# Optimization experiments

Hardware: AMD Instinct MI355X
Metric: run time of the kernel (lower is better)

## Reference

```python
import jax, jax.numpy as jnp
import numpy as np

B, N, D_IN, D_OUT = 8, 2048, 256, 256
BN_EPS = 1e-5
SELU_ALPHA = 1.6732632423543772
SELU_SCALE = 1.0507009873554805


def setup_inputs() -> dict:
    key = jax.random.key(0)
    k1, k2, k3, k4 = jax.random.split(key, 4)
    lim_lin = 1.0 / np.sqrt(D_IN)
    return {
        "x": jax.random.normal(k1, (B, N, D_IN), dtype=jnp.float32),
        "w_map": jax.random.uniform(k2, (D_IN,), jnp.float32, -lim_lin, lim_lin),
        "w_att": jax.random.uniform(k3, (D_OUT, D_IN), jnp.float32, -lim_lin, lim_lin),
        "w_res": jax.random.uniform(k4, (D_OUT, D_IN), jnp.float32, -lim_lin, lim_lin),
        "gamma": jnp.ones((D_OUT,), jnp.float32),
        "beta": jnp.zeros((D_OUT,), jnp.float32),
    }


def _selu(x):
    x_clamped = jnp.clip(x, -10.0, 10.0)
    return SELU_SCALE * jnp.where(x > 0, x, SELU_ALPHA * (jnp.exp(x_clamped) - 1.0))


def reference(x, w_map, w_att, w_res, gamma, beta):
    # scores[b,i,j] = sum_d w_map[d] * x[b,i,d] * x[b,j,d]  (== W_map(x_i*x_j))
    scores = jnp.einsum("bid,bjd->bij", x * w_map, x)  # [B,N,N]
    attn = jax.nn.softmax(scores, axis=-1)
    aggregated = jnp.einsum("bij,bjd->bid", attn, x)  # [B,N,D]
    out = aggregated @ w_att.T + x @ w_res.T  # [B,N,D_OUT]
    # BatchNorm1d in training mode: stats over (batch, nodes) per channel, biased var
    mean = jnp.mean(out, axis=(0, 1))
    var = jnp.mean(jnp.square(out - mean), axis=(0, 1))
    out = (out - mean) * jax.lax.rsqrt(var + BN_EPS) * gamma + beta
    return _selu(out)
```

## Files before the change

kernel.cpp:

```cpp
#include <hip/hip_runtime.h>
#include <hip/hip_bf16.h>


typedef __attribute__((ext_vector_type(8)))  short bf16x8;
typedef __attribute__((ext_vector_type(4)))  float f32x4;
typedef __attribute__((ext_vector_type(16))) float f32x16;

#define MFMA16(a, b, c) __builtin_amdgcn_mfma_f32_16x16x32_bf16((a), (b), (c), 0, 0, 0)
#define MFMA32(a, b, c) __builtin_amdgcn_mfma_f32_32x32x16_bf16((a), (b), (c), 0, 0, 0)

constexpr int   NB = 8, NN = 2048;
constexpr int   ROWS = NB * NN;
constexpr float BN_EPS = 1e-5f;
constexpr float SELU_ALPHA = 1.6732632423543772f;
constexpr float SELU_SCALE = 1.0507009873554805f;

__device__ __forceinline__ unsigned short f2bf(float f) {
  union { float f; unsigned int u; } v; v.f = f;
  unsigned int u = v.u;
  u += 0x7FFFu + ((u >> 16) & 1u);
  return (unsigned short)(u >> 16);
}
__device__ __forceinline__ float bf2f(unsigned short h) {
  union { float f; unsigned int u; } v; v.u = ((unsigned int)h) << 16;
  return v.f;
}
__device__ __forceinline__ unsigned int pk2(float lo, float hi) {
  return (unsigned int)f2bf(lo) | ((unsigned int)f2bf(hi) << 16);
}

__device__ __forceinline__ void async_copy16(const unsigned short* g, unsigned short* l) {
  __builtin_amdgcn_global_load_lds(
      (const __attribute__((address_space(1))) void*)g,
      (__attribute__((address_space(3))) void*)l, 16, 0, 0);
}

__global__ __launch_bounds__(256) void k0_prep(const float* __restrict__ x,
                                               unsigned short* __restrict__ XR,
                                               unsigned short* __restrict__ Xt,
                                               const float* __restrict__ w_att,
                                               const float* __restrict__ w_res,
                                               unsigned short* __restrict__ WC,
                                               float* __restrict__ sums) {
  __shared__ unsigned short Ls[64 * 264];
  const int t = threadIdx.x;
  const int b = blockIdx.x & 7, rt = blockIdx.x >> 3;
  const int grb = b * NN + rt * 64;
  const int c = (t & 31) * 8, r0 = t >> 5;
#pragma unroll
  for (int q = 0; q < 8; ++q) {
    int r = r0 + q * 8;
    const float* xp = x + (size_t)(grb + r) * 256 + c;
    float4 a = *(const float4*)xp;
    float4 d = *(const float4*)(xp + 4);
    union { unsigned short s[8]; uint4 v; } xb;
    xb.s[0] = f2bf(a.x); xb.s[1] = f2bf(a.y); xb.s[2] = f2bf(a.z); xb.s[3] = f2bf(a.w);
    xb.s[4] = f2bf(d.x); xb.s[5] = f2bf(d.y); xb.s[6] = f2bf(d.z); xb.s[7] = f2bf(d.w);
    *(uint4*)(XR + (size_t)(grb + r) * 256 + c) = xb.v;
    *(uint4*)&Ls[r * 264 + c] = xb.v;
  }
  __syncthreads();
  unsigned short* dst = Xt + ((size_t)b * 256 + t) * 2048 + rt * 64;
#pragma unroll
  for (int k = 0; k < 8; ++k) {
    union { unsigned short s[8]; uint4 v; } o;
#pragma unroll
    for (int j = 0; j < 8; ++j) o.s[j] = Ls[(k * 8 + j) * 264 + t];
    *(uint4*)(dst + k * 8) = o.v;
  }
  if (blockIdx.x == 0 && t < 256) ((float4*)sums)[t] = make_float4(0.f, 0.f, 0.f, 0.f);
  if (blockIdx.x < 64) {
    int f = (blockIdx.x * 256 + t) * 8;
    int cc = f >> 9, k = f & 511;
    const float* src = (k < 256) ? (w_att + cc * 256 + k) : (w_res + cc * 256 + (k - 256));
    float4 a = *(const float4*)src;
    float4 d = *(const float4*)(src + 4);
    union { unsigned short s[8]; uint4 v; } o;
    o.s[0] = f2bf(a.x); o.s[1] = f2bf(a.y); o.s[2] = f2bf(a.z); o.s[3] = f2bf(a.w);
    o.s[4] = f2bf(d.x); o.s[5] = f2bf(d.y); o.s[6] = f2bf(d.z); o.s[7] = f2bf(d.w);
    *(uint4*)(WC + f) = o.v;
  }
}

__global__ __launch_bounds__(512, 2) void k1_attn(const float* __restrict__ w_map,
                                                  const unsigned short* __restrict__ XR,
                                                  const unsigned short* __restrict__ Xt,
                                                  unsigned short* __restrict__ Opart,
                                                  float* __restrict__ Lpart) {
  __shared__ unsigned short Ks[2][32 * 256];
  __shared__ unsigned short Vt[2][256 * 32];

  const int t = threadIdx.x;
  const int w = t >> 6, lane = t & 63;
  const int l31 = lane & 31, h = lane >> 5;
  const int qb = blockIdx.x >> 2, p = blockIdx.x & 3;
  const int b = qb >> 3;
  const int rowbase = qb * 256;
  const int jb0 = b * 2048 + p * 512;
  const unsigned short* Xtb = Xt + (size_t)b * 256 * 2048;

  int kSrc[2], vSrc[2];
#pragma unroll
  for (int q = 0; q < 2; ++q) {
    int cch = q * 512 + t;
    int kj = cch >> 5, kck = cch & 31;
    int pj = ((kj >> 3) & 1) * 16 + ((kj >> 4) & 1) * 4 + (kj & 3) + ((kj >> 2) & 1) * 8;
    kSrc[q] = (jb0 + pj) * 256 + ((kck ^ (kj & 7)) * 8);
    int vd = cch >> 2, vcj = cch & 3;
    vSrc[q] = vd * 2048 + p * 512 + ((vcj ^ ((vd >> 1) & 3)) * 8);
  }

#pragma unroll
  for (int q = 0; q < 2; ++q)
    async_copy16(XR + kSrc[q], &Ks[0][(q * 512 + t) * 8]);
#pragma unroll
  for (int q = 0; q < 2; ++q)
    async_copy16(Xtb + vSrc[q], &Vt[0][(q * 512 + t) * 8]);

  bf16x8 qf[16];
  {
    const unsigned short* xrow = XR + (size_t)(rowbase + w * 32 + l31) * 256 + h * 8;
#pragma unroll
    for (int kc = 0; kc < 16; ++kc) {
      bf16x8 xb = *(const bf16x8*)(xrow + kc * 16);
      const float* wp = w_map + kc * 16 + h * 8;
      float4 w0 = *(const float4*)wp, w1 = *(const float4*)(wp + 4);
      float wv[8] = {w0.x, w0.y, w0.z, w0.w, w1.x, w1.y, w1.z, w1.w};
      bf16x8 qv;
#pragma unroll
      for (int i = 0; i < 8; ++i)
        qv[i] = (short)f2bf(bf2f((unsigned short)xb[i]) * wv[i]);
      qf[kc] = qv;
    }
  }

  const f32x16 fz16 = {0.f,0.f,0.f,0.f, 0.f,0.f,0.f,0.f, 0.f,0.f,0.f,0.f, 0.f,0.f,0.f,0.f};
  f32x16 oacc[8];
#pragma unroll
  for (int i = 0; i < 8; ++i) oacc[i] = fz16;
  float rsum = 0.f;

  const int sw7 = l31 & 7;
  const int vkey = (l31 >> 1) & 3;

  for (int jt = 0; jt < 16; ++jt) {
    const int cur = jt & 1;
    __syncthreads();
    if (jt < 15) {
#pragma unroll
      for (int q = 0; q < 2; ++q)
        async_copy16(XR + kSrc[q] + (jt + 1) * 8192, &Ks[cur ^ 1][(q * 512 + t) * 8]);
#pragma unroll
      for (int q = 0; q < 2; ++q)
        async_copy16(Xtb + vSrc[q] + (jt + 1) * 32, &Vt[cur ^ 1][(q * 512 + t) * 8]);
    }
    f32x16 sA = fz16, sB = fz16;
#pragma unroll
    for (int kc = 0; kc < 8; ++kc) {
      bf16x8 kf = *(const bf16x8*)&Ks[cur][l31 * 256 + (((2 * kc + h) ^ sw7) * 8)];
      sA = MFMA32(kf, qf[kc], sA);
    }
#pragma unroll
    for (int kc = 8; kc < 16; ++kc) {
      bf16x8 kf = *(const bf16x8*)&Ks[cur][l31 * 256 + (((2 * kc + h) ^ sw7) * 8)];
      sB = MFMA32(kf, qf[kc], sB);
    }
    float pv[16];
#pragma unroll
    for (int r = 0; r < 16; ++r) {
      pv[r] = __expf(sA[r] + sB[r]);
      rsum += pv[r];
    }
    union { unsigned int u[4]; bf16x8 v; } a0, a1;
    a0.u[0] = pk2(pv[0],  pv[1]);
    a0.u[1] = pk2(pv[2],  pv[3]);
    a0.u[2] = pk2(pv[8],  pv[9]);
    a0.u[3] = pk2(pv[10], pv[11]);
    a1.u[0] = pk2(pv[4],  pv[5]);
    a1.u[1] = pk2(pv[6],  pv[7]);
    a1.u[2] = pk2(pv[12], pv[13]);
    a1.u[3] = pk2(pv[14], pv[15]);
#pragma unroll
    for (int dt = 0; dt < 8; ++dt) {
      const int dbase = (dt * 32 + l31) * 32;
      bf16x8 v0 = *(const bf16x8*)&Vt[cur][dbase + ((h ^ vkey) * 8)];
      oacc[dt] = MFMA32(a0.v, v0, oacc[dt]);
      bf16x8 v1 = *(const bf16x8*)&Vt[cur][dbase + (((2 + h) ^ vkey) * 8)];
      oacc[dt] = MFMA32(a1.v, v1, oacc[dt]);
    }
  }

  float rsT = rsum + __shfl_xor(rsum, 32);
  if (h == 0) Lpart[(size_t)p * ROWS + rowbase + w * 32 + l31] = rsT;
  unsigned short* ob = Opart + ((size_t)p * ROWS + rowbase + w * 32) * 256 + l31;
#pragma unroll
  for (int dt = 0; dt < 8; ++dt)
#pragma unroll
    for (int r = 0; r < 16; ++r) {
      int qrow = (r & 3) + ((r >> 2) << 3) + (h << 2);
      ob[qrow * 256 + dt * 32] = f2bf(oacc[dt][r]);
    }
}

__global__ __launch_bounds__(256) void kc_comb(const unsigned short* __restrict__ Opart,
                                               const float* __restrict__ Lpart,
                                               unsigned short* __restrict__ Oagg) {
  const int t = threadIdx.x;
  const int row = blockIdx.x * 8 + (t >> 5);
  const int col = (t & 31) * 8;
  const float invL = 1.0f / (Lpart[row] + Lpart[ROWS + row] +
                             Lpart[2 * ROWS + row] + Lpart[3 * ROWS + row]);
  const size_t base = (size_t)row * 256 + col;
  union { unsigned short s[8]; uint4 v; } p0, p1, p2, p3, o;
  p0.v = *(const uint4*)(Opart + base);
  p1.v = *(const uint4*)(Opart + (size_t)ROWS * 256 + base);
  p2.v = *(const uint4*)(Opart + (size_t)2 * ROWS * 256 + base);
  p3.v = *(const uint4*)(Opart + (size_t)3 * ROWS * 256 + base);
#pragma unroll
  for (int e = 0; e < 8; ++e)
    o.s[e] = f2bf(((bf2f(p0.s[e]) + bf2f(p1.s[e])) + (bf2f(p2.s[e]) + bf2f(p3.s[e]))) * invL);
  *(uint4*)(Oagg + base) = o.v;
}

__global__ __launch_bounds__(256, 2) void k2_gemm(const unsigned short* __restrict__ XR,
                                                  const unsigned short* __restrict__ Oagg,
                                                  const unsigned short* __restrict__ WC,
                                                  float* __restrict__ out,
                                                  float* __restrict__ sums) {
  __shared__ unsigned short As[128 * 72];
  __shared__ unsigned short Bs[64 * 72];
  __shared__ float cs[64], cq[64];
  const int t = threadIdx.x;
  const int w = t >> 6, lane = t & 63, l15 = lane & 15, quad = lane >> 4;
  const int m0 = (blockIdx.x >> 2) * 128, n0 = (blockIdx.x & 3) * 64;
  if (t < 64) { cs[t] = 0.f; cq[t] = 0.f; }

  const f32x4 fz = {0.f, 0.f, 0.f, 0.f};
  f32x4 acc[4][2];
#pragma unroll
  for (int i = 0; i < 4; ++i) { acc[i][0] = fz; acc[i][1] = fz; }

  for (int kk = 0; kk < 512; kk += 64) {
    __syncthreads();
#pragma unroll
    for (int q = 0; q < 4; ++q) {
      int idx = t + q * 256;
      int row = idx >> 3, koff = (idx & 7) * 8;
      const unsigned short* src = (kk < 256)
          ? (Oagg + (size_t)(m0 + row) * 256 + kk + koff)
          : (XR + (size_t)(m0 + row) * 256 + (kk - 256) + koff);
      *(uint4*)&As[row * 72 + koff] = *(const uint4*)src;
    }
#pragma unroll
    for (int q = 0; q < 2; ++q) {
      int idx = t + q * 256;
      int row = idx >> 3, koff = (idx & 7) * 8;
      *(uint4*)&Bs[row * 72 + koff] = *(const uint4*)(WC + (size_t)(n0 + row) * 512 + kk + koff);
    }
    __syncthreads();
#pragma unroll
    for (int kc = 0; kc < 2; ++kc) {
      bf16x8 b0 = *(const bf16x8*)&Bs[((w >> 1) * 32 + l15) * 72 + kc * 32 + quad * 8];
      bf16x8 b1 = *(const bf16x8*)&Bs[((w >> 1) * 32 + 16 + l15) * 72 + kc * 32 + quad * 8];
#pragma unroll
      for (int mt = 0; mt < 4; ++mt) {
        bf16x8 af = *(const bf16x8*)&As[((w & 1) * 64 + mt * 16 + l15) * 72 + kc * 32 + quad * 8];
        acc[mt][0] = MFMA16(af, b0, acc[mt][0]);
        acc[mt][1] = MFMA16(af, b1, acc[mt][1]);
      }
    }
  }
#pragma unroll
  for (int mt = 0; mt < 4; ++mt)
#pragma unroll
    for (int nt = 0; nt < 2; ++nt)
#pragma unroll
      for (int r = 0; r < 4; ++r) {
        int grow = m0 + (w & 1) * 64 + mt * 16 + quad * 4 + r;
        int gcol = n0 + (w >> 1) * 32 + nt * 16 + l15;
        out[(size_t)grow * 256 + gcol] = acc[mt][nt][r];
      }
#pragma unroll
  for (int nt = 0; nt < 2; ++nt) {
    float a = 0.f, b2 = 0.f;
#pragma unroll
    for (int mt = 0; mt < 4; ++mt)
#pragma unroll
      for (int r = 0; r < 4; ++r) {
        float v = acc[mt][nt][r];
        a += v; b2 += v * v;
      }
    a += __shfl_xor(a, 16);  a += __shfl_xor(a, 32);
    b2 += __shfl_xor(b2, 16); b2 += __shfl_xor(b2, 32);
    if (quad == 0) {
      int ci = (w >> 1) * 32 + nt * 16 + l15;
      atomicAdd(&cs[ci], a);
      atomicAdd(&cq[ci], b2);
    }
  }
  __syncthreads();
  if (t < 64) {
    atomicAdd(&sums[n0 + t], cs[t]);
    atomicAdd(&sums[256 + n0 + t], cq[t]);
  }
}

__global__ __launch_bounds__(256) void k4_bn_selu(float* __restrict__ out,
                                                  const float* __restrict__ sums,
                                                  const float* __restrict__ gamma,
                                                  const float* __restrict__ beta) {
  int f = (blockIdx.x * 256 + threadIdx.x) * 8;
  int c = f & 255;
  const float inv_m = 1.0f / 16384.0f;
  float4 v0 = *(const float4*)(out + f);
  float4 v1 = *(const float4*)(out + f + 4);
  float vv[8] = {v0.x, v0.y, v0.z, v0.w, v1.x, v1.y, v1.z, v1.w};
#pragma unroll
  for (int k = 0; k < 8; ++k) {
    int ch = c + k;
    float mean = sums[ch] * inv_m;
    float var = sums[256 + ch] * inv_m - mean * mean;
    float y = (vv[k] - mean) * rsqrtf(var + BN_EPS) * gamma[ch] + beta[ch];
    float yc = fminf(fmaxf(y, -10.f), 10.f);
    float r = (y > 0.f) ? y : (SELU_ALPHA * (expf(yc) - 1.0f));
    vv[k] = SELU_SCALE * r;
  }
  float4 o0 = {vv[0], vv[1], vv[2], vv[3]};
  float4 o1 = {vv[4], vv[5], vv[6], vv[7]};
  *(float4*)(out + f) = o0;
  *(float4*)(out + f + 4) = o1;
}

extern "C" void kernel_launch(void* const* d_in, const int* in_sizes, int n_in,
                              void* d_out, int out_size, void* d_ws, size_t ws_size,
                              hipStream_t stream) {
  const float* x     = (const float*)d_in[0];
  const float* w_map = (const float*)d_in[1];
  const float* w_att = (const float*)d_in[2];
  const float* w_res = (const float*)d_in[3];
  const float* gamma = (const float*)d_in[4];
  const float* beta  = (const float*)d_in[5];
  float* out = (float*)d_out;

  unsigned short* XR = (unsigned short*)d_ws;
  unsigned short* Xt = XR + (size_t)ROWS * 256;
  unsigned short* WC = Xt + (size_t)NB * 256 * 2048;
  unsigned short* Opart = WC + 256 * 512;
  float* Lpart = (float*)(Opart + (size_t)4 * ROWS * 256);
  float* sums  = Lpart + 4 * ROWS;
  unsigned short* Oagg = Xt;

  k0_prep<<<256, 256, 0, stream>>>(x, XR, Xt, w_att, w_res, WC, sums);
  k1_attn<<<256, 512, 0, stream>>>(w_map, XR, Xt, Opart, Lpart);
  kc_comb<<<2048, 256, 0, stream>>>(Opart, Lpart, Oagg);
  k2_gemm<<<512, 256, 0, stream>>>(XR, Oagg, WC, out, sums);
  k4_bn_selu<<<2048, 256, 0, stream>>>(out, sums, gamma, beta);
}
```

Before: 163.0 us.

## Fuse partial-combine and BatchNorm+SELU into GEMM with grid-wide barrier

Removes the separate combine kernel: the GEMM now sums the four attention partials and applies the 1/L normalisation while loading its A tile. It also removes the separate BN+SELU kernel by having every block publish column statistics with global atomics, wait at a grid-wide spin barrier on a counter, then normalise and apply SELU in registers before a single write of the output. This avoids writing and re-reading the aggregated activations and the fp32 pre-activation output, and drops two launches. The GEMM tile becomes 64 rows by all 256 columns, so W is reloaded per block. The spin barrier relies on all 256 blocks being co-resident and on the counter being reset before each call, which the visible code does not show.

After: 177.8 us. 1.09x slower.

```diff
diff --git a/kernel.cpp b/kernel.cpp
--- a/kernel.cpp
+++ b/kernel.cpp
@@ -202,86 +202,86 @@
     }
 }
 
-__global__ __launch_bounds__(256) void kc_comb(const unsigned short* __restrict__ Opart,
-                                               const float* __restrict__ Lpart,
-                                               unsigned short* __restrict__ Oagg) {
-  const int t = threadIdx.x;
-  const int row = blockIdx.x * 8 + (t >> 5);
-  const int col = (t & 31) * 8;
-  const float invL = 1.0f / (Lpart[row] + Lpart[ROWS + row] +
-                             Lpart[2 * ROWS + row] + Lpart[3 * ROWS + row]);
-  const size_t base = (size_t)row * 256 + col;
-  union { unsigned short s[8]; uint4 v; } p0, p1, p2, p3, o;
-  p0.v = *(const uint4*)(Opart + base);
-  p1.v = *(const uint4*)(Opart + (size_t)ROWS * 256 + base);
-  p2.v = *(const uint4*)(Opart + (size_t)2 * ROWS * 256 + base);
-  p3.v = *(const uint4*)(Opart + (size_t)3 * ROWS * 256 + base);
-#pragma unroll
-  for (int e = 0; e < 8; ++e)
-    o.s[e] = f2bf(((bf2f(p0.s[e]) + bf2f(p1.s[e])) + (bf2f(p2.s[e]) + bf2f(p3.s[e]))) * invL);
-  *(uint4*)(Oagg + base) = o.v;
-}
-
 __global__ __launch_bounds__(256, 2) void k2_gemm(const unsigned short* __restrict__ XR,
-                                                  const unsigned short* __restrict__ Oagg,
+                                                  const unsigned short* __restrict__ Opart,
+                                                  const float* __restrict__ Lpart,
                                                   const unsigned short* __restrict__ WC,
                                                   float* __restrict__ out,
-                                                  float* __restrict__ sums) {
-  __shared__ unsigned short As[128 * 72];
-  __shared__ unsigned short Bs[64 * 72];
-  __shared__ float cs[64], cq[64];
+                                                  float* __restrict__ sums,
+                                                  const float* __restrict__ gamma,
+                                                  const float* __restrict__ beta) {
+  __shared__ unsigned short As[64 * 72];
+  __shared__ unsigned short Bs[256 * 72];
+  __shared__ float invLs[64];
   const int t = threadIdx.x;
   const int w = t >> 6, lane = t & 63, l15 = lane & 15, quad = lane >> 4;
-  const int m0 = (blockIdx.x >> 2) * 128, n0 = (blockIdx.x & 3) * 64;
-  if (t < 64) { cs[t] = 0.f; cq[t] = 0.f; }
+  const int m0 = blockIdx.x * 64;
+  if (t < 64) {
+    int row = m0 + t;
+    invLs[t] = 1.0f / (Lpart[row] + Lpart[ROWS + row] +
+                       Lpart[2 * ROWS + row] + Lpart[3 * ROWS + row]);
+  }
 
   const f32x4 fz = {0.f, 0.f, 0.f, 0.f};
-  f32x4 acc[4][2];
-#pragma unroll
-  for (int i = 0; i < 4; ++i) { acc[i][0] = fz; acc[i][1] = fz; }
+  f32x4 acc[4][4];
+#pragma unroll
+  for (int i = 0; i < 4; ++i)
+#pragma unroll
+    for (int j = 0; j < 4; ++j) acc[i][j] = fz;
 
   for (int kk = 0; kk < 512; kk += 64) {
     __syncthreads();
-#pragma unroll
-    for (int q = 0; q < 4; ++q) {
-      int idx = t + q * 256;
+    if (kk < 256) {
+#pragma unroll
+      for (int i = 0; i < 2; ++i) {
+        int idx = t + i * 256;
+        int row = idx >> 3, koff = (idx & 7) * 8;
+        size_t base = (size_t)(m0 + row) * 256 + kk + koff;
+        union { unsigned short s[8]; uint4 v; } p0, p1, p2, p3, o;
+        p0.v = *(const uint4*)(Opart + base);
+        p1.v = *(const uint4*)(Opart + (size_t)ROWS * 256 + base);
+        p2.v = *(const uint4*)(Opart + (size_t)2 * ROWS * 256 + base);
+        p3.v = *(const uint4*)(Opart + (size_t)3 * ROWS * 256 + base);
+        float il = invLs[row];
+#pragma unroll
+        for (int e = 0; e < 8; ++e)
+          o.s[e] = f2bf(((bf2f(p0.s[e]) + bf2f(p1.s[e])) +
+                         (bf2f(p2.s[e]) + bf2f(p3.s[e]))) * il);
+        *(uint4*)&As[row * 72 + koff] = o.v;
+      }
+    } else {
+#pragma unroll
+      for (int i = 0; i < 2; ++i) {
+        int idx = t + i * 256;
+        int row = idx >> 3, koff = (idx & 7) * 8;
+        *(uint4*)&As[row * 72 + koff] =
+            *(const uint4*)(XR + (size_t)(m0 + row) * 256 + (kk - 256) + koff);
+      }
+    }
+#pragma unroll
+    for (int i = 0; i < 8; ++i) {
+      int idx = t + i * 256;
       int row = idx >> 3, koff = (idx & 7) * 8;
-      const unsigned short* src = (kk < 256)
-          ? (Oagg + (size_t)(m0 + row) * 256 + kk + koff)
-          : (XR + (size_t)(m0 + row) * 256 + (kk - 256) + koff);
-      *(uint4*)&As[row * 72 + koff] = *(const uint4*)src;
-    }
-#pragma unroll
-    for (int q = 0; q < 2; ++q) {
-      int idx = t + q * 256;
-      int row = idx >> 3, koff = (idx & 7) * 8;
-      *(uint4*)&Bs[row * 72 + koff] = *(const uint4*)(WC + (size_t)(n0 + row) * 512 + kk + koff);
+      *(uint4*)&Bs[row * 72 + koff] = *(const uint4*)(WC + (size_t)row * 512 + kk + koff);
     }
     __syncthreads();
 #pragma unroll
     for (int kc = 0; kc < 2; ++kc) {
-      bf16x8 b0 = *(const bf16x8*)&Bs[((w >> 1) * 32 + l15) * 72 + kc * 32 + quad * 8];
-      bf16x8 b1 = *(const bf16x8*)&Bs[((w >> 1) * 32 + 16 + l15) * 72 + kc * 32 + quad * 8];
-#pragma unroll
-      for (int mt = 0; mt < 4; ++mt) {
-        bf16x8 af = *(const bf16x8*)&As[((w & 1) * 64 + mt * 16 + l15) * 72 + kc * 32 + quad * 8];
-        acc[mt][0] = MFMA16(af, b0, acc[mt][0]);
-        acc[mt][1] = MFMA16(af, b1, acc[mt][1]);
-      }
-    }
-  }
-#pragma unroll
-  for (int mt = 0; mt < 4; ++mt)
-#pragma unroll
-    for (int nt = 0; nt < 2; ++nt)
-#pragma unroll
-      for (int r = 0; r < 4; ++r) {
-        int grow = m0 + (w & 1) * 64 + mt * 16 + quad * 4 + r;
-        int gcol = n0 + (w >> 1) * 32 + nt * 16 + l15;
-        out[(size_t)grow * 256 + gcol] = acc[mt][nt][r];
-      }
-#pragma unroll
-  for (int nt = 0; nt < 2; ++nt) {
+      bf16x8 af[4];
+#pragma unroll
+      for (int mt = 0; mt < 4; ++mt)
+        af[mt] = *(const bf16x8*)&As[(mt * 16 + l15) * 72 + kc * 32 + quad * 8];
+#pragma unroll
+      for (int nt = 0; nt < 4; ++nt) {
+        bf16x8 bf = *(const bf16x8*)&Bs[(w * 64 + nt * 16 + l15) * 72 + kc * 32 + quad * 8];
+#pragma unroll
+        for (int mt = 0; mt < 4; ++mt)
+          acc[mt][nt] = MFMA16(af[mt], bf, acc[mt][nt]);
+      }
+    }
+  }
+#pragma unroll
+  for (int nt = 0; nt < 4; ++nt) {
     float a = 0.f, b2 = 0.f;
 #pragma unroll
     for (int mt = 0; mt < 4; ++mt)
@@ -293,42 +293,41 @@
     a += __shfl_xor(a, 16);  a += __shfl_xor(a, 32);
     b2 += __shfl_xor(b2, 16); b2 += __shfl_xor(b2, 32);
     if (quad == 0) {
-      int ci = (w >> 1) * 32 + nt * 16 + l15;
-      atomicAdd(&cs[ci], a);
-      atomicAdd(&cq[ci], b2);
-    }
-  }
+      int col = w * 64 + nt * 16 + l15;
+      atomicAdd(&sums[col], a);
+      atomicAdd(&sums[256 + col], b2);
+    }
+  }
+  __threadfence();
   __syncthreads();
-  if (t < 64) {
-    atomicAdd(&sums[n0 + t], cs[t]);
-    atomicAdd(&sums[256 + n0 + t], cq[t]);
-  }
-}
-
-__global__ __launch_bounds__(256) void k4_bn_selu(float* __restrict__ out,
-                                                  const float* __restrict__ sums,
-                                                  const float* __restrict__ gamma,
-                                                  const float* __restrict__ beta) {
-  int f = (blockIdx.x * 256 + threadIdx.x) * 8;
-  int c = f & 255;
+  int* cnt = (int*)(sums + 512);
+  if (t == 0) {
+    atomicAdd(cnt, 1);
+    while (__hip_atomic_load(cnt, __ATOMIC_ACQUIRE, __HIP_MEMORY_SCOPE_AGENT) < 256)
+      __builtin_amdgcn_s_sleep(8);
+  }
+  __syncthreads();
   const float inv_m = 1.0f / 16384.0f;
-  float4 v0 = *(const float4*)(out + f);
-  float4 v1 = *(const float4*)(out + f + 4);
-  float vv[8] = {v0.x, v0.y, v0.z, v0.w, v1.x, v1.y, v1.z, v1.w};
-#pragma unroll
-  for (int k = 0; k < 8; ++k) {
-    int ch = c + k;
-    float mean = sums[ch] * inv_m;
-    float var = sums[256 + ch] * inv_m - mean * mean;
-    float y = (vv[k] - mean) * rsqrtf(var + BN_EPS) * gamma[ch] + beta[ch];
-    float yc = fminf(fmaxf(y, -10.f), 10.f);
-    float r = (y > 0.f) ? y : (SELU_ALPHA * (expf(yc) - 1.0f));
-    vv[k] = SELU_SCALE * r;
-  }
-  float4 o0 = {vv[0], vv[1], vv[2], vv[3]};
-  float4 o1 = {vv[4], vv[5], vv[6], vv[7]};
-  *(float4*)(out + f) = o0;
-  *(float4*)(out + f + 4) = o1;
+#pragma unroll
+  for (int nt = 0; nt < 4; ++nt) {
+    int col = w * 64 + nt * 16 + l15;
+    float sm = __hip_atomic_load(&sums[col], __ATOMIC_RELAXED, __HIP_MEMORY_SCOPE_AGENT);
+    float sq = __hip_atomic_load(&sums[256 + col], __ATOMIC_RELAXED, __HIP_MEMORY_SCOPE_AGENT);
+    float mean = sm * inv_m;
+    float var = sq * inv_m - mean * mean;
+    float sc = rsqrtf(var + BN_EPS) * gamma[col];
+    float bi = beta[col] - mean * sc;
+#pragma unroll
+    for (int mt = 0; mt < 4; ++mt)
+#pragma unroll
+      for (int r = 0; r < 4; ++r) {
+        int grow = m0 + mt * 16 + quad * 4 + r;
+        float y = acc[mt][nt][r] * sc + bi;
+        float yc = fminf(fmaxf(y, -10.f), 10.f);
+        float rr = (y > 0.f) ? y : (SELU_ALPHA * (expf(yc) - 1.0f));
+        out[(size_t)grow * 256 + col] = SELU_SCALE * rr;
+      }
+  }
 }
 
 extern "C" void kernel_launch(void* const* d_in, const int* in_sizes, int n_in,
@@ -348,11 +347,8 @@
   unsigned short* Opart = WC + 256 * 512;
   float* Lpart = (float*)(Opart + (size_t)4 * ROWS * 256);
   float* sums  = Lpart + 4 * ROWS;
-  unsigned short* Oagg = Xt;
 
   k0_prep<<<256, 256, 0, stream>>>(x, XR, Xt, w_att, w_res, WC, sums);
   k1_attn<<<256, 512, 0, stream>>>(w_map, XR, Xt, Opart, Lpart);
-  kc_comb<<<2048, 256, 0, stream>>>(Opart, Lpart, Oagg);
-  k2_gemm<<<512, 256, 0, stream>>>(XR, Oagg, WC, out, sums);
-  k4_bn_selu<<<2048, 256, 0, stream>>>(out, sums, gamma, beta);
-}
+  k2_gemm<<<256, 256, 0, stream>>>(XR, Opart, Lpart, WC, out, sums, gamma, beta);
+}
```

## Software-pipeline QK^T and PV across tiles with triple-buffered V in attention kernel

Applied to the files above, without the earlier changes.

Restructures the attention loop so the score MFMAs for tile j+1 are issued alongside the PV MFMAs for tile j, with the exp/pack of the new scores placed after the PV work. K stays double-buffered and V becomes triple-buffered, with a two-tile-ahead prefetch and a prologue/epilogue. The aim is to hide the exp/softmax latency and the MFMA dependency chains behind independent matrix work. The cost is more LDS (an extra V buffer), which may hurt occupancy at 2 blocks per CU, plus more live registers.

Result: slower. 172.6 us (+5.9%).

```diff
diff --git a/kernel.cpp b/kernel.cpp
--- a/kernel.cpp
+++ b/kernel.cpp
@@ -88,7 +88,7 @@
                                                   unsigned short* __restrict__ Opart,
                                                   float* __restrict__ Lpart) {
   __shared__ unsigned short Ks[2][32 * 256];
-  __shared__ unsigned short Vt[2][256 * 32];
+  __shared__ unsigned short Vt[3][256 * 32];
 
   const int t = threadIdx.x;
   const int w = t >> 6, lane = t & 63;
@@ -111,11 +111,15 @@
   }
 
 #pragma unroll
-  for (int q = 0; q < 2; ++q)
+  for (int q = 0; q < 2; ++q) {
     async_copy16(XR + kSrc[q], &Ks[0][(q * 512 + t) * 8]);
-#pragma unroll
-  for (int q = 0; q < 2; ++q)
+    async_copy16(XR + kSrc[q] + 8192, &Ks[1][(q * 512 + t) * 8]);
+  }
+#pragma unroll
+  for (int q = 0; q < 2; ++q) {
     async_copy16(Xtb + vSrc[q], &Vt[0][(q * 512 + t) * 8]);
+    async_copy16(Xtb + vSrc[q] + 32, &Vt[1][(q * 512 + t) * 8]);
+  }
 
   bf16x8 qf[16];
   {
@@ -143,50 +147,85 @@
   const int sw7 = l31 & 7;
   const int vkey = (l31 >> 1) & 3;
 
-  for (int jt = 0; jt < 16; ++jt) {
-    const int cur = jt & 1;
+  __syncthreads();
+
+  bf16x8 afA, afB;
+  {
+    f32x16 sA = fz16, sB = fz16;
+#pragma unroll
+    for (int kc = 0; kc < 8; ++kc) {
+      bf16x8 kf = *(const bf16x8*)&Ks[0][l31 * 256 + (((2 * kc + h) ^ sw7) * 8)];
+      sA = MFMA32(kf, qf[kc], sA);
+    }
+#pragma unroll
+    for (int kc = 8; kc < 16; ++kc) {
+      bf16x8 kf = *(const bf16x8*)&Ks[0][l31 * 256 + (((2 * kc + h) ^ sw7) * 8)];
+      sB = MFMA32(kf, qf[kc], sB);
+    }
+    float pv[16];
+#pragma unroll
+    for (int r = 0; r < 16; ++r) { pv[r] = __expf(sA[r] + sB[r]); rsum += pv[r]; }
+    union { unsigned int u[4]; bf16x8 v; } a0, a1;
+    a0.u[0] = pk2(pv[0],  pv[1]);  a0.u[1] = pk2(pv[2],  pv[3]);
+    a0.u[2] = pk2(pv[8],  pv[9]);  a0.u[3] = pk2(pv[10], pv[11]);
+    a1.u[0] = pk2(pv[4],  pv[5]);  a1.u[1] = pk2(pv[6],  pv[7]);
+    a1.u[2] = pk2(pv[12], pv[13]); a1.u[3] = pk2(pv[14], pv[15]);
+    afA = a0.v; afB = a1.v;
+  }
+
+  int v_cur = 0, v_nxt = 1, v_dma = 2;
+
+  for (int jt = 0; jt < 15; ++jt) {
     __syncthreads();
-    if (jt < 15) {
+    if (jt < 14) {
 #pragma unroll
       for (int q = 0; q < 2; ++q)
-        async_copy16(XR + kSrc[q] + (jt + 1) * 8192, &Ks[cur ^ 1][(q * 512 + t) * 8]);
+        async_copy16(XR + kSrc[q] + (jt + 2) * 8192, &Ks[jt & 1][(q * 512 + t) * 8]);
 #pragma unroll
       for (int q = 0; q < 2; ++q)
-        async_copy16(Xtb + vSrc[q] + (jt + 1) * 32, &Vt[cur ^ 1][(q * 512 + t) * 8]);
-    }
+        async_copy16(Xtb + vSrc[q] + (jt + 2) * 32, &Vt[v_dma][(q * 512 + t) * 8]);
+    }
+    const unsigned short* Kb = &Ks[(jt + 1) & 1][0];
     f32x16 sA = fz16, sB = fz16;
 #pragma unroll
     for (int kc = 0; kc < 8; ++kc) {
-      bf16x8 kf = *(const bf16x8*)&Ks[cur][l31 * 256 + (((2 * kc + h) ^ sw7) * 8)];
+      bf16x8 kf = *(const bf16x8*)&Kb[l31 * 256 + (((2 * kc + h) ^ sw7) * 8)];
       sA = MFMA32(kf, qf[kc], sA);
     }
 #pragma unroll
     for (int kc = 8; kc < 16; ++kc) {
-      bf16x8 kf = *(const bf16x8*)&Ks[cur][l31 * 256 + (((2 * kc + h) ^ sw7) * 8)];
+      bf16x8 kf = *(const bf16x8*)&Kb[l31 * 256 + (((2 * kc + h) ^ sw7) * 8)];
       sB = MFMA32(kf, qf[kc], sB);
     }
-    float pv[16];
-#pragma unroll
-    for (int r = 0; r < 16; ++r) {
-      pv[r] = __expf(sA[r] + sB[r]);
-      rsum += pv[r];
-    }
-    union { unsigned int u[4]; bf16x8 v; } a0, a1;
-    a0.u[0] = pk2(pv[0],  pv[1]);
-    a0.u[1] = pk2(pv[2],  pv[3]);
-    a0.u[2] = pk2(pv[8],  pv[9]);
-    a0.u[3] = pk2(pv[10], pv[11]);
-    a1.u[0] = pk2(pv[4],  pv[5]);
-    a1.u[1] = pk2(pv[6],  pv[7]);
-    a1.u[2] = pk2(pv[12], pv[13]);
-    a1.u[3] = pk2(pv[14], pv[15]);
+    const unsigned short* Vb = &Vt[v_cur][0];
 #pragma unroll
     for (int dt = 0; dt < 8; ++dt) {
       const int dbase = (dt * 32 + l31) * 32;
-      bf16x8 v0 = *(const bf16x8*)&Vt[cur][dbase + ((h ^ vkey) * 8)];
-      oacc[dt] = MFMA32(a0.v, v0, oacc[dt]);
-      bf16x8 v1 = *(const bf16x8*)&Vt[cur][dbase + (((2 + h) ^ vkey) * 8)];
-      oacc[dt] = MFMA32(a1.v, v1, oacc[dt]);
+      bf16x8 v0 = *(const bf16x8*)&Vb[dbase + ((h ^ vkey) * 8)];
+      oacc[dt] = MFMA32(afA, v0, oacc[dt]);
+      bf16x8 v1 = *(const bf16x8*)&Vb[dbase + (((2 + h) ^ vkey) * 8)];
+      oacc[dt] = MFMA32(afB, v1, oacc[dt]);
+    }
+    float pv[16];
+#pragma unroll
+    for (int r = 0; r < 16; ++r) { pv[r] = __expf(sA[r] + sB[r]); rsum += pv[r]; }
+    union { unsigned int u[4]; bf16x8 v; } a0, a1;
+    a0.u[0] = pk2(pv[0],  pv[1]);  a0.u[1] = pk2(pv[2],  pv[3]);
+    a0.u[2] = pk2(pv[8],  pv[9]);  a0.u[3] = pk2(pv[10], pv[11]);
+    a1.u[0] = pk2(pv[4],  pv[5]);  a1.u[1] = pk2(pv[6],  pv[7]);
+    a1.u[2] = pk2(pv[12], pv[13]); a1.u[3] = pk2(pv[14], pv[15]);
+    afA = a0.v; afB = a1.v;
+    int tmp = v_cur; v_cur = v_nxt; v_nxt = v_dma; v_dma = tmp;
+  }
+  {
+    const unsigned short* Vb = &Vt[v_cur][0];
+#pragma unroll
+    for (int dt = 0; dt < 8; ++dt) {
+      const int dbase = (dt * 32 + l31) * 32;
+      bf16x8 v0 = *(const bf16x8*)&Vb[dbase + ((h ^ vkey) * 8)];
+      oacc[dt] = MFMA32(afA, v0, oacc[dt]);
+      bf16x8 v1 = *(const bf16x8*)&Vb[dbase + (((2 + h) ^ vkey) * 8)];
+      oacc[dt] = MFMA32(afB, v1, oacc[dt]);
     }
   }
 
```
